# Optimization experiments

Measured on AMD Instinct MI355X. Metric: run time of the kernel, lower is better.

Reference implementation:

```python
import jax, jax.numpy as jnp
import numpy as np

B, H, W, C = 16, 56, 56, 256
K = 3          # ikernel
G = 8          # group
C4 = C // 4    # ratio=4
EPS = 1e-5


def setup_inputs() -> dict:
    key = jax.random.key(0)
    ks = jax.random.split(key, 16)
    s = lambda *sh: 1.0 / np.sqrt(sh[-1])
    inp = {
        'x': jax.random.normal(ks[0], (B, H, W, C), jnp.float32),
        # Involution: conv1 (C->C4, 1x1), BN affine, conv2 (C4 -> G*K*K, 1x1)
        'conv1_w': jax.random.normal(ks[1], (C4, C), jnp.float32) * s(C4, C),
        'conv1_b': jnp.zeros((C4,), jnp.float32),
        'bn_gamma': jnp.ones((C4,), jnp.float32),
        'bn_beta': jnp.zeros((C4,), jnp.float32),
        'conv2_w': jax.random.normal(ks[2], (G * K * K, C4), jnp.float32) * s(G * K * K, C4),
        'conv2_b': jnp.zeros((G * K * K,), jnp.float32),
        # mlp_c: Linear(dim, dim, bias=False)
        'mlp_c_w': jax.random.normal(ks[3], (C, C), jnp.float32) * s(C, C),
        # reweight1: Mlp(dim, dim//4, dim*2)
        'fc1_w': jax.random.normal(ks[4], (C4, C), jnp.float32) * s(C4, C),
        'fc1_b': jnp.zeros((C4,), jnp.float32),
        'fc2_w': jax.random.normal(ks[5], (2 * C, C4), jnp.float32) * s(2 * C, C4),
        'fc2_b': jnp.zeros((2 * C,), jnp.float32),
        # projcnn: Conv2d(dim, dim, 1)
        'projcnn_w': jax.random.normal(ks[6], (C, C), jnp.float32) * s(C, C),
        'projcnn_b': jnp.zeros((C,), jnp.float32),
    }
    return inp


def _involution(x, conv1_w, conv1_b, bn_gamma, bn_beta, conv2_w, conv2_b):
    # x: [B,H,W,C] (channels-last equivalent of the torch NCHW path)
    # kernel-generating branch: 1x1 conv -> BN (batch stats, training mode) -> relu -> 1x1 conv
    t = jnp.einsum('bhwc,oc->bhwo', x, conv1_w) + conv1_b          # [B,H,W,C4]
    mu = t.mean(axis=(0, 1, 2))
    var = t.var(axis=(0, 1, 2))
    t = jax.nn.relu(bn_gamma * (t - mu) * jax.lax.rsqrt(var + EPS) + bn_beta)
    w = jnp.einsum('bhwc,oc->bhwo', t, conv2_w) + conv2_b          # [B,H,W,G*K*K]
    w = w.reshape(B, H, W, G, K * K)
    # unfold: pad and stack the K*K shifted views (row-major kernel order, matches torch)
    p = K // 2
    xp = jnp.pad(x, ((0, 0), (p, p), (p, p), (0, 0)))
    patches = jnp.stack([xp[:, i:i + H, j:j + W, :] for i in range(K) for j in range(K)],
                        axis=3)                                     # [B,H,W,KK,C]
    patches = patches.reshape(B, H, W, K * K, G, C // G)
    out = jnp.einsum('bhwkgc,bhwgk->bhwgc', patches, w)             # multiply + sum over kernel dim
    return out.reshape(B, H, W, C)


def reference(x, conv1_w, conv1_b, bn_gamma, bn_beta, conv2_w, conv2_b,
              mlp_c_w, fc1_w, fc1_b, fc2_w, fc2_b, projcnn_w, projcnn_b):
    hw = _involution(x, conv1_w, conv1_b, bn_gamma, bn_beta, conv2_w, conv2_b)  # [B,H,W,C]
    c = jnp.einsum('bhwc,oc->bhwo', x, mlp_c_w)                                  # [B,H,W,C]
    a = (hw + c).mean(axis=(1, 2))                                               # [B,C]
    a = jax.nn.gelu(jnp.einsum('bc,oc->bo', a, fc1_w) + fc1_b, approximate=False)
    a = jnp.einsum('bc,oc->bo', a, fc2_w) + fc2_b                                # [B,2C]
    a = a.reshape(B, C, 2).transpose(2, 0, 1)                                    # [2,B,C]
    a = jax.nn.softmax(a, axis=0)[:, :, None, None, :]                           # [2,B,1,1,C]
    y = hw * a[0] + c * a[1]
    return jnp.einsum('bhwc,oc->bhwo', y, projcnn_w) + projcnn_b
```

## Files before the change

### kernel.cpp

```cpp
#include <hip/hip_runtime.h>
#include <math.h>

#define BB 16
#define HH 56
#define WW 56
#define CC 256
#define O2P 80
#define NPIX 50176
#define HWP 3136

typedef __attribute__((ext_vector_type(4))) float f32x4;
typedef __attribute__((ext_vector_type(8))) short bh8;
typedef __attribute__((ext_vector_type(4))) short bh4;

__device__ inline short f2bf(float f) {
    union { float f; unsigned u; } v; v.f = f;
    unsigned r = (v.u + 0x7fffu + ((v.u >> 16) & 1u)) >> 16;
    return (short)r;
}
__device__ inline float bf2f(short s) {
    union { unsigned u; float f; } v; v.u = ((unsigned)(unsigned short)s) << 16;
    return v.f;
}

__device__ inline void stage_tile(const short* __restrict__ src, int rowBase, int ldk,
                                  int kc, char* smem, int nchunks, int wid, int lane)
{
    for (int ci = wid; ci < nchunks; ci += 4) {
        int row = ci * 8 + (lane >> 3);
        int cb = (lane & 7) ^ (row & 7);
        const short* gp = src + (size_t)(rowBase + row) * ldk + kc + cb * 8;
        __builtin_amdgcn_global_load_lds(
            (const __attribute__((address_space(1))) void*)gp,
            (__attribute__((address_space(3))) void*)(smem + ci * 1024), 16, 0, 0);
    }
}

template<int BN, int AMODE, int OUTBF>
__global__ __launch_bounds__(256) void mgemm(
    const short* __restrict__ Ab,
    const float* __restrict__ Af, const float* __restrict__ scsh,
    const short* __restrict__ Ah, const short* __restrict__ Ac,
    const float* __restrict__ g0, const float* __restrict__ g1,
    const short* __restrict__ Wb, const float* __restrict__ bias,
    void* __restrict__ outp, int K, int O, int ldOut)
{
    constexpr int WN = (BN == 128) ? 2 : 1;
    constexpr int MR = (BN == 128) ? 4 : 2;
    constexpr int NR = BN / (16 * WN);
    constexpr int BCH = BN / 8;

    __shared__ alignas(16) char smA[16384];
    __shared__ alignas(16) char smB[BN * 128];

    const int tid = threadIdx.x;
    const int lane = tid & 63, wid = tid >> 6;
    const int rowBase = blockIdx.x * 128;
    const int ocBase = blockIdx.y * BN;
    const int waveM = (BN == 128) ? (wid >> 1) * 64 : wid * 32;
    const int waveN = (BN == 128) ? (wid & 1) * 64 : 0;

    f32x4 acc[MR][NR];
    #pragma unroll
    for (int m = 0; m < MR; ++m)
        #pragma unroll
        for (int n = 0; n < NR; ++n) acc[m][n] = f32x4{0.f, 0.f, 0.f, 0.f};

    for (int kc = 0; kc < K; kc += 64) {
        if constexpr (AMODE == 0) {
            stage_tile(Ab, rowBase, K, kc, smA, 16, wid, lane);
        } else if constexpr (AMODE == 1) {
            #pragma unroll
            for (int q = tid; q < 2048; q += 256) {
                int row = q >> 4, k4 = (q & 15) * 4;
                f32x4 v = *(const f32x4*)(Af + (size_t)(rowBase + row) * K + kc + k4);
                bh4 o;
                #pragma unroll
                for (int j = 0; j < 4; ++j) {
                    float sc = scsh[kc + k4 + j], sh = scsh[64 + kc + k4 + j];
                    o[j] = f2bf(fmaxf(v[j] * sc + sh, 0.f));
                }
                int byt = row * 128 + (((k4 >> 3) ^ (row & 7)) << 4) + (k4 & 7) * 2;
                *(bh4*)(smA + byt) = o;
            }
        } else {
            #pragma unroll
            for (int q = tid; q < 1024; q += 256) {
                int row = q >> 3, cb = q & 7;
                int n = rowBase + row;
                int b = n / HWP;
                const size_t off = (size_t)n * 256 + kc + cb * 8;
                bh8 h8 = *(const bh8*)(Ah + off);
                bh8 c8 = *(const bh8*)(Ac + off);
                bh8 o;
                #pragma unroll
                for (int j = 0; j < 8; ++j) {
                    float w0 = g0[b * 256 + kc + cb * 8 + j];
                    float w1 = g1[b * 256 + kc + cb * 8 + j];
                    o[j] = f2bf(bf2f(h8[j]) * w0 + bf2f(c8[j]) * w1);
                }
                *(bh8*)(smA + row * 128 + ((cb ^ (row & 7)) << 4)) = o;
            }
        }
        stage_tile(Wb, ocBase, K, kc, smB, BCH, wid, lane);
        __syncthreads();

        #pragma unroll
        for (int ks = 0; ks < 2; ++ks) {
            bh8 aF[MR], bF[NR];
            #pragma unroll
            for (int m = 0; m < MR; ++m) {
                int r = waveM + m * 16 + (lane & 15);
                int cb = ks * 4 + (lane >> 4);
                aF[m] = *(const bh8*)(smA + r * 128 + ((cb ^ (r & 7)) << 4));
            }
            #pragma unroll
            for (int n = 0; n < NR; ++n) {
                int r = waveN + n * 16 + (lane & 15);
                int cb = ks * 4 + (lane >> 4);
                bF[n] = *(const bh8*)(smB + r * 128 + ((cb ^ (r & 7)) << 4));
            }
            #pragma unroll
            for (int m = 0; m < MR; ++m)
                #pragma unroll
                for (int n = 0; n < NR; ++n)
                    acc[m][n] = __builtin_amdgcn_mfma_f32_16x16x32_bf16(
                        aF[m], bF[n], acc[m][n], 0, 0, 0);
        }
        __syncthreads();
    }

    #pragma unroll
    for (int m = 0; m < MR; ++m)
        #pragma unroll
        for (int n = 0; n < NR; ++n)
            #pragma unroll
            for (int j = 0; j < 4; ++j) {
                int r = rowBase + waveM + m * 16 + (lane >> 4) * 4 + j;
                int c = ocBase + waveN + n * 16 + (lane & 15);
                if (c < O) {
                    float v = acc[m][n][j] + (bias ? bias[c] : 0.f);
                    if constexpr (OUTBF)
                        ((short*)outp)[(size_t)r * ldOut + c] = f2bf(v);
                    else
                        ((float*)outp)[(size_t)r * ldOut + c] = v;
                }
            }
}

__global__ __launch_bounds__(256) void cvt_x_kernel(const float* __restrict__ x,
                                                    short* __restrict__ xb)
{
    size_t i = ((size_t)blockIdx.x * 256 + threadIdx.x) * 8;
    f32x4 v0 = *(const f32x4*)(x + i);
    f32x4 v1 = *(const f32x4*)(x + i + 4);
    bh8 o;
    #pragma unroll
    for (int j = 0; j < 4; ++j) { o[j] = f2bf(v0[j]); o[4 + j] = f2bf(v1[j]); }
    *(bh8*)(xb + i) = o;
}

__global__ __launch_bounds__(256) void cvt_w_kernel(
    const float* __restrict__ c1, const float* __restrict__ mc,
    const float* __restrict__ pj, const float* __restrict__ c2,
    short* __restrict__ c1b, short* __restrict__ mcb,
    short* __restrict__ pjb, short* __restrict__ c2b)
{
    int i = blockIdx.x * 256 + threadIdx.x;
    if (i < 16384) c1b[i] = f2bf(c1[i]);
    if (i < 65536) { mcb[i] = f2bf(mc[i]); pjb[i] = f2bf(pj[i]); }
    if (i < O2P * 64) {
        int o = i >> 6, k = i & 63;
        c2b[i] = (o < 72) ? f2bf(c2[o * 64 + k]) : (short)0;
    }
}

__global__ __launch_bounds__(256) void bn_stats_kernel(
    const float* __restrict__ t, float* __restrict__ stats)
{
    __shared__ float ps[4][64], pq[4][64];
    const int tid = threadIdx.x;
    const int ch = tid & 63, rg = tid >> 6;
    const size_t base = (size_t)blockIdx.x * 512;
    float s = 0.f, q = 0.f;
    for (int r = rg; r < 512; r += 4) {
        float v = t[(base + r) * 64 + ch];
        s += v; q += v * v;
    }
    ps[rg][ch] = s; pq[rg][ch] = q;
    __syncthreads();
    if (rg == 0) {
        atomicAdd(&stats[ch],      ps[0][ch] + ps[1][ch] + ps[2][ch] + ps[3][ch]);
        atomicAdd(&stats[64 + ch], pq[0][ch] + pq[1][ch] + pq[2][ch] + pq[3][ch]);
    }
}

__global__ void bn_finalize_kernel(
    const float* __restrict__ stats, const float* __restrict__ gamma,
    const float* __restrict__ beta, float* __restrict__ scsh)
{
    int ch = threadIdx.x;
    const float invN = 1.f / (float)NPIX;
    float mean = stats[ch] * invN;
    float var  = stats[64 + ch] * invN - mean * mean;
    float sc = gamma[ch] * rsqrtf(var + 1e-5f);
    scsh[ch] = sc;
    scsh[64 + ch] = beta[ch] - mean * sc;
}

__global__ __launch_bounds__(256) void invol_kernel(
    const float* __restrict__ x, const float* __restrict__ wmat,
    short* __restrict__ hwb)
{
    const int bh = blockIdx.x;
    const int b = bh / HH, h = bh % HH;
    const int c = threadIdx.x;
    const int g = c >> 5;
    const float* xb_ = x + (size_t)b * HWP * CC + c;

    float c0[3], c1[3], c2[3];
    auto loadcol = [&](int W, float* dst) {
        if (W < 0 || W >= WW) { dst[0] = dst[1] = dst[2] = 0.f; return; }
        #pragma unroll
        for (int i = 0; i < 3; ++i) {
            int hh = h + i - 1;
            dst[i] = (hh < 0 || hh >= HH) ? 0.f : xb_[((size_t)hh * WW + W) * CC];
        }
    };
    loadcol(-1, c0);
    loadcol(0, c1);
    for (int w = 0; w < WW; ++w) {
        loadcol(w + 1, c2);
        const int n = bh * WW + w;
        const float* wr = wmat + (size_t)n * O2P + g * 9;
        float acc = c0[0] * wr[0] + c1[0] * wr[1] + c2[0] * wr[2]
                  + c0[1] * wr[3] + c1[1] * wr[4] + c2[1] * wr[5]
                  + c0[2] * wr[6] + c1[2] * wr[7] + c2[2] * wr[8];
        hwb[(size_t)n * CC + c] = f2bf(acc);
        c0[0] = c1[0]; c0[1] = c1[1]; c0[2] = c1[2];
        c1[0] = c2[0]; c1[1] = c2[1]; c1[2] = c2[2];
    }
}

__global__ __launch_bounds__(256) void mean_kernel(
    const short* __restrict__ hwb, const short* __restrict__ cmb,
    float* __restrict__ asum)
{
    const int b = blockIdx.x, s = blockIdx.y;
    const int c = threadIdx.x;
    const int base = b * HWP + s * (HWP / 8);
    float acc = 0.f;
    for (int p = 0; p < HWP / 8; ++p) {
        size_t idx = (size_t)(base + p) * CC + c;
        acc += bf2f(hwb[idx]) + bf2f(cmb[idx]);
    }
    atomicAdd(&asum[b * CC + c], acc);
}

__global__ __launch_bounds__(256) void mlp_kernel(
    const float* __restrict__ asum,
    const float* __restrict__ fc1_w, const float* __restrict__ fc1_b,
    const float* __restrict__ fc2_w, const float* __restrict__ fc2_b,
    float* __restrict__ a0, float* __restrict__ a1)
{
    __shared__ float a[256], hbuf[64], f[512];
    const int b = blockIdx.x, tid = threadIdx.x;
    a[tid] = asum[b * CC + tid] * (1.f / (float)HWP);
    __syncthreads();
    if (tid < 64) {
        float s = fc1_b[tid];
        for (int c = 0; c < 256; ++c) s += a[c] * fc1_w[tid * 256 + c];
        hbuf[tid] = 0.5f * s * (1.f + erff(s * 0.7071067811865476f));
    }
    __syncthreads();
    for (int o = tid; o < 512; o += 256) {
        float s = fc2_b[o];
        for (int c = 0; c < 64; ++c) s += hbuf[c] * fc2_w[o * 64 + c];
        f[o] = s;
    }
    __syncthreads();
    float f0 = f[2 * tid], f1 = f[2 * tid + 1];
    float m = fmaxf(f0, f1);
    float e0 = expf(f0 - m), e1 = expf(f1 - m);
    float inv = 1.f / (e0 + e1);
    a0[b * CC + tid] = e0 * inv;
    a1[b * CC + tid] = e1 * inv;
}

extern "C" void kernel_launch(void* const* d_in, const int* in_sizes, int n_in,
                              void* d_out, int out_size, void* d_ws, size_t ws_size,
                              hipStream_t stream)
{
    (void)in_sizes; (void)n_in; (void)out_size; (void)ws_size;
    const float* x        = (const float*)d_in[0];
    const float* conv1_w  = (const float*)d_in[1];
    const float* conv1_b  = (const float*)d_in[2];
    const float* bn_gamma = (const float*)d_in[3];
    const float* bn_beta  = (const float*)d_in[4];
    const float* conv2_w  = (const float*)d_in[5];
    const float* conv2_b  = (const float*)d_in[6];
    const float* mlp_c_w  = (const float*)d_in[7];
    const float* fc1_w    = (const float*)d_in[8];
    const float* fc1_b    = (const float*)d_in[9];
    const float* fc2_w    = (const float*)d_in[10];
    const float* fc2_b    = (const float*)d_in[11];
    const float* projcnn_w= (const float*)d_in[12];
    const float* projcnn_b= (const float*)d_in[13];
    float* out = (float*)d_out;

    char* p = (char*)d_ws;
    short* xb  = (short*)p; p += (size_t)NPIX * 256 * 2;
    short* hwb = (short*)p; p += (size_t)NPIX * 256 * 2;
    short* cmb = (short*)p;
    float* t   = (float*)cmb;
    p += (size_t)NPIX * 256 * 2;
    float* wmat = (float*)p; p += (size_t)NPIX * O2P * 4;
    short* c1b = (short*)p; p += 64 * 256 * 2;
    short* mcb = (short*)p; p += 256 * 256 * 2;
    short* pjb = (short*)p; p += 256 * 256 * 2;
    short* c2b = (short*)p; p += O2P * 64 * 2;
    float* stats = (float*)p; p += 128 * 4;
    float* asum  = (float*)p; p += BB * 256 * 4;
    float* scsh  = (float*)p; p += 128 * 4;
    float* a0    = (float*)p; p += BB * 256 * 4;
    float* a1    = (float*)p; p += BB * 256 * 4;

    hipMemsetAsync(stats, 0, (128 + BB * 256) * sizeof(float), stream);

    cvt_x_kernel<<<NPIX * 256 / (256 * 8), 256, 0, stream>>>(x, xb);
    cvt_w_kernel<<<256, 256, 0, stream>>>(conv1_w, mlp_c_w, projcnn_w, conv2_w,
                                          c1b, mcb, pjb, c2b);
    mgemm<64, 0, 0><<<dim3(392, 1), 256, 0, stream>>>(
        xb, nullptr, nullptr, nullptr, nullptr, nullptr, nullptr,
        c1b, conv1_b, t, 256, 64, 64);
    bn_stats_kernel<<<98, 256, 0, stream>>>(t, stats);
    bn_finalize_kernel<<<1, 64, 0, stream>>>(stats, bn_gamma, bn_beta, scsh);
    mgemm<O2P, 1, 0><<<dim3(392, 1), 256, 0, stream>>>(
        nullptr, t, scsh, nullptr, nullptr, nullptr, nullptr,
        c2b, conv2_b, wmat, 64, 72, O2P);
    invol_kernel<<<BB * HH, 256, 0, stream>>>(x, wmat, hwb);
    mgemm<128, 0, 1><<<dim3(392, 2), 256, 0, stream>>>(
        xb, nullptr, nullptr, nullptr, nullptr, nullptr, nullptr,
        mcb, nullptr, cmb, 256, 256, 256);
    mean_kernel<<<dim3(BB, 8), 256, 0, stream>>>(hwb, cmb, asum);
    mlp_kernel<<<BB, 256, 0, stream>>>(asum, fc1_w, fc1_b, fc2_w, fc2_b, a0, a1);
    mgemm<128, 2, 0><<<dim3(392, 2), 256, 0, stream>>>(
        nullptr, nullptr, nullptr, hwb, cmb, a0, a1,
        pjb, projcnn_b, out, 256, 256, 256);
}
```

Measured before the change: 337.4 us.

## Fuse channel means into conversion and involution, store intermediates in bf16

Removes the separate mean pass over hwb and cmb. The per-batch mean of the mlp_c branch is now computed algebraically from per-batch sums of x, taken during the bf16 conversion and multiplied by mlp_c_w inside the MLP kernel. The involution mean is accumulated inside a restructured involution kernel, which now reads bf16 x and bf16 kernel weights and handles 4 channels per thread over half-row blocks. The conv1 output t and the generated kernels wmat are stored in bf16 rather than fp32, cutting intermediate traffic at the cost of some precision and extra atomics.

Result: faster. 296.4 us (-12.2%).

```diff
diff --git a/kernel.cpp b/kernel.cpp
--- a/kernel.cpp
+++ b/kernel.cpp
@@ -39,7 +39,7 @@
 template<int BN, int AMODE, int OUTBF>
 __global__ __launch_bounds__(256) void mgemm(
     const short* __restrict__ Ab,
-    const float* __restrict__ Af, const float* __restrict__ scsh,
+    const short* __restrict__ At, const float* __restrict__ scsh,
     const short* __restrict__ Ah, const short* __restrict__ Ac,
     const float* __restrict__ g0, const float* __restrict__ g1,
     const short* __restrict__ Wb, const float* __restrict__ bias,
@@ -71,17 +71,16 @@
             stage_tile(Ab, rowBase, K, kc, smA, 16, wid, lane);
         } else if constexpr (AMODE == 1) {
             #pragma unroll
-            for (int q = tid; q < 2048; q += 256) {
-                int row = q >> 4, k4 = (q & 15) * 4;
-                f32x4 v = *(const f32x4*)(Af + (size_t)(rowBase + row) * K + kc + k4);
-                bh4 o;
+            for (int q = tid; q < 1024; q += 256) {
+                int row = q >> 3, cb = q & 7;
+                bh8 v = *(const bh8*)(At + (size_t)(rowBase + row) * K + kc + cb * 8);
+                bh8 o;
                 #pragma unroll
-                for (int j = 0; j < 4; ++j) {
-                    float sc = scsh[kc + k4 + j], sh = scsh[64 + kc + k4 + j];
-                    o[j] = f2bf(fmaxf(v[j] * sc + sh, 0.f));
+                for (int j = 0; j < 8; ++j) {
+                    int k = kc + cb * 8 + j;
+                    o[j] = f2bf(fmaxf(bf2f(v[j]) * scsh[k] + scsh[64 + k], 0.f));
                 }
-                int byt = row * 128 + (((k4 >> 3) ^ (row & 7)) << 4) + (k4 & 7) * 2;
-                *(bh4*)(smA + byt) = o;
+                *(bh8*)(smA + row * 128 + ((cb ^ (row & 7)) << 4)) = o;
             }
         } else {
             #pragma unroll
@@ -149,15 +148,33 @@
 }
 
 __global__ __launch_bounds__(256) void cvt_x_kernel(const float* __restrict__ x,
-                                                    short* __restrict__ xb)
-{
-    size_t i = ((size_t)blockIdx.x * 256 + threadIdx.x) * 8;
-    f32x4 v0 = *(const f32x4*)(x + i);
-    f32x4 v1 = *(const f32x4*)(x + i + 4);
+                                                    short* __restrict__ xb,
+                                                    float* __restrict__ sxb)
+{
+    __shared__ float sm[8][256];
+    const int tid = threadIdx.x;
+    size_t base = (size_t)blockIdx.x * 2048 + tid * 8;
+    const int b = (int)(base >> 8) / HWP;
+    const int ch0 = (int)(base & 255);
+    const int pix = (tid * 8) >> 8;
+
+    f32x4 v0 = *(const f32x4*)(x + base);
+    f32x4 v1 = *(const f32x4*)(x + base + 4);
     bh8 o;
     #pragma unroll
     for (int j = 0; j < 4; ++j) { o[j] = f2bf(v0[j]); o[4 + j] = f2bf(v1[j]); }
-    *(bh8*)(xb + i) = o;
+    *(bh8*)(xb + base) = o;
+
+    #pragma unroll
+    for (int j = 0; j < 4; ++j) {
+        sm[pix][ch0 + j] = v0[j];
+        sm[pix][ch0 + 4 + j] = v1[j];
+    }
+    __syncthreads();
+    float s = 0.f;
+    #pragma unroll
+    for (int p = 0; p < 8; ++p) s += sm[p][tid];
+    atomicAdd(&sxb[b * CC + tid], s);
 }
 
 __global__ __launch_bounds__(256) void cvt_w_kernel(
@@ -176,22 +193,30 @@
 }
 
 __global__ __launch_bounds__(256) void bn_stats_kernel(
-    const float* __restrict__ t, float* __restrict__ stats)
-{
-    __shared__ float ps[4][64], pq[4][64];
+    const short* __restrict__ t, float* __restrict__ stats)
+{
+    __shared__ float ss[32][64], sq[32][64];
     const int tid = threadIdx.x;
-    const int ch = tid & 63, rg = tid >> 6;
-    const size_t base = (size_t)blockIdx.x * 512;
-    float s = 0.f, q = 0.f;
-    for (int r = rg; r < 512; r += 4) {
-        float v = t[(base + r) * 64 + ch];
-        s += v; q += v * v;
-    }
-    ps[rg][ch] = s; pq[rg][ch] = q;
-    __syncthreads();
-    if (rg == 0) {
-        atomicAdd(&stats[ch],      ps[0][ch] + ps[1][ch] + ps[2][ch] + ps[3][ch]);
-        atomicAdd(&stats[64 + ch], pq[0][ch] + pq[1][ch] + pq[2][ch] + pq[3][ch]);
+    const int grp = tid >> 3, ch0 = (tid & 7) * 8;
+    const size_t rowBase = (size_t)blockIdx.x * 512;
+    float s[8] = {}, q[8] = {};
+    for (int r = grp; r < 512; r += 32) {
+        bh8 v = *(const bh8*)(t + (rowBase + r) * 64 + ch0);
+        #pragma unroll
+        for (int j = 0; j < 8; ++j) {
+            float f = bf2f(v[j]);
+            s[j] += f; q[j] += f * f;
+        }
+    }
+    #pragma unroll
+    for (int j = 0; j < 8; ++j) { ss[grp][ch0 + j] = s[j]; sq[grp][ch0 + j] = q[j]; }
+    __syncthreads();
+    if (tid < 64) {
+        float ts = 0.f, tq = 0.f;
+        #pragma unroll
+        for (int g = 0; g < 32; ++g) { ts += ss[g][tid]; tq += sq[g][tid]; }
+        atomicAdd(&stats[tid], ts);
+        atomicAdd(&stats[64 + tid], tq);
     }
 }
 
@@ -209,63 +234,80 @@
 }
 
 __global__ __launch_bounds__(256) void invol_kernel(
-    const float* __restrict__ x, const float* __restrict__ wmat,
-    short* __restrict__ hwb)
-{
-    const int bh = blockIdx.x;
+    const short* __restrict__ xb, const short* __restrict__ wmatb,
+    short* __restrict__ hwb, float* __restrict__ asum)
+{
+    __shared__ float sm4[4][256];
+    const int idx = blockIdx.x;
+    const int s = idx & 1, bh = idx >> 1;
     const int b = bh / HH, h = bh % HH;
-    const int c = threadIdx.x;
-    const int g = c >> 5;
-    const float* xb_ = x + (size_t)b * HWP * CC + c;
-
-    float c0[3], c1[3], c2[3];
-    auto loadcol = [&](int W, float* dst) {
-        if (W < 0 || W >= WW) { dst[0] = dst[1] = dst[2] = 0.f; return; }
+    const int tid = threadIdx.x;
+    const int lane = tid & 63, wid = tid >> 6;
+    const int c4 = lane * 4;
+    const int g = lane >> 3;
+    const int w0 = s * 28 + wid * 7;
+    const short* xbase = xb + ((size_t)b * HWP) * CC + c4;
+
+    float cL[3][4], cM[3][4], cR[3][4];
+    auto loadcol = [&](int Wc, float d[3][4]) {
         #pragma unroll
         for (int i = 0; i < 3; ++i) {
             int hh = h + i - 1;
-            dst[i] = (hh < 0 || hh >= HH) ? 0.f : xb_[((size_t)hh * WW + W) * CC];
+            if (Wc < 0 || Wc >= WW || hh < 0 || hh >= HH) {
+                d[i][0] = d[i][1] = d[i][2] = d[i][3] = 0.f;
+            } else {
+                bh4 v = *(const bh4*)(xbase + (size_t)(hh * WW + Wc) * CC);
+                #pragma unroll
+                for (int j = 0; j < 4; ++j) d[i][j] = bf2f(v[j]);
+            }
         }
     };
-    loadcol(-1, c0);
-    loadcol(0, c1);
-    for (int w = 0; w < WW; ++w) {
-        loadcol(w + 1, c2);
+    loadcol(w0 - 1, cL);
+    loadcol(w0, cM);
+
+    float loc[4] = {0.f, 0.f, 0.f, 0.f};
+    for (int w = w0; w < w0 + 7; ++w) {
+        loadcol(w + 1, cR);
         const int n = bh * WW + w;
-        const float* wr = wmat + (size_t)n * O2P + g * 9;
-        float acc = c0[0] * wr[0] + c1[0] * wr[1] + c2[0] * wr[2]
-                  + c0[1] * wr[3] + c1[1] * wr[4] + c2[1] * wr[5]
-                  + c0[2] * wr[6] + c1[2] * wr[7] + c2[2] * wr[8];
-        hwb[(size_t)n * CC + c] = f2bf(acc);
-        c0[0] = c1[0]; c0[1] = c1[1]; c0[2] = c1[2];
-        c1[0] = c2[0]; c1[1] = c2[1]; c1[2] = c2[2];
-    }
-}
-
-__global__ __launch_bounds__(256) void mean_kernel(
-    const short* __restrict__ hwb, const short* __restrict__ cmb,
-    float* __restrict__ asum)
-{
-    const int b = blockIdx.x, s = blockIdx.y;
-    const int c = threadIdx.x;
-    const int base = b * HWP + s * (HWP / 8);
-    float acc = 0.f;
-    for (int p = 0; p < HWP / 8; ++p) {
-        size_t idx = (size_t)(base + p) * CC + c;
-        acc += bf2f(hwb[idx]) + bf2f(cmb[idx]);
-    }
-    atomicAdd(&asum[b * CC + c], acc);
+        const short* wr = wmatb + (size_t)n * O2P + g * 9;
+        float wf[9];
+        #pragma unroll
+        for (int t9 = 0; t9 < 9; ++t9) wf[t9] = bf2f(wr[t9]);
+        bh4 ov;
+        #pragma unroll
+        for (int j = 0; j < 4; ++j) {
+            float a = cL[0][j] * wf[0] + cM[0][j] * wf[1] + cR[0][j] * wf[2]
+                    + cL[1][j] * wf[3] + cM[1][j] * wf[4] + cR[1][j] * wf[5]
+                    + cL[2][j] * wf[6] + cM[2][j] * wf[7] + cR[2][j] * wf[8];
+            loc[j] += a;
+            ov[j] = f2bf(a);
+        }
+        *(bh4*)(hwb + (size_t)n * CC + c4) = ov;
+        #pragma unroll
+        for (int i = 0; i < 3; ++i)
+            #pragma unroll
+            for (int j = 0; j < 4; ++j) { cL[i][j] = cM[i][j]; cM[i][j] = cR[i][j]; }
+    }
+    #pragma unroll
+    for (int j = 0; j < 4; ++j) sm4[wid][c4 + j] = loc[j];
+    __syncthreads();
+    float tot = sm4[0][tid] + sm4[1][tid] + sm4[2][tid] + sm4[3][tid];
+    atomicAdd(&asum[b * CC + tid], tot);
 }
 
 __global__ __launch_bounds__(256) void mlp_kernel(
-    const float* __restrict__ asum,
+    const float* __restrict__ asum, const float* __restrict__ sxb,
+    const float* __restrict__ mlp_c_w,
     const float* __restrict__ fc1_w, const float* __restrict__ fc1_b,
     const float* __restrict__ fc2_w, const float* __restrict__ fc2_b,
     float* __restrict__ a0, float* __restrict__ a1)
 {
     __shared__ float a[256], hbuf[64], f[512];
     const int b = blockIdx.x, tid = threadIdx.x;
-    a[tid] = asum[b * CC + tid] * (1.f / (float)HWP);
+    float acm = 0.f;
+    const float* wrow = mlp_c_w + (size_t)tid * 256;
+    for (int c = 0; c < 256; ++c) acm += sxb[b * CC + c] * wrow[c];
+    a[tid] = (asum[b * CC + tid] + acm) * (1.f / (float)HWP);
     __syncthreads();
     if (tid < 64) {
         float s = fc1_b[tid];
@@ -312,38 +354,39 @@
     short* xb  = (short*)p; p += (size_t)NPIX * 256 * 2;
     short* hwb = (short*)p; p += (size_t)NPIX * 256 * 2;
     short* cmb = (short*)p;
-    float* t   = (float*)cmb;
+    short* t   = (short*)cmb;
     p += (size_t)NPIX * 256 * 2;
-    float* wmat = (float*)p; p += (size_t)NPIX * O2P * 4;
+    short* wmatb = (short*)p; p += (size_t)NPIX * O2P * 2;
     short* c1b = (short*)p; p += 64 * 256 * 2;
     short* mcb = (short*)p; p += 256 * 256 * 2;
     short* pjb = (short*)p; p += 256 * 256 * 2;
     short* c2b = (short*)p; p += O2P * 64 * 2;
     float* stats = (float*)p; p += 128 * 4;
     float* asum  = (float*)p; p += BB * 256 * 4;
+    float* sxb   = (float*)p; p += BB * 256 * 4;
     float* scsh  = (float*)p; p += 128 * 4;
     float* a0    = (float*)p; p += BB * 256 * 4;
     float* a1    = (float*)p; p += BB * 256 * 4;
 
-    hipMemsetAsync(stats, 0, (128 + BB * 256) * sizeof(float), stream);
-
-    cvt_x_kernel<<<NPIX * 256 / (256 * 8), 256, 0, stream>>>(x, xb);
+    hipMemsetAsync(stats, 0, (128 + 2 * BB * 256) * sizeof(float), stream);
+
+    cvt_x_kernel<<<NPIX * 256 / 2048, 256, 0, stream>>>(x, xb, sxb);
     cvt_w_kernel<<<256, 256, 0, stream>>>(conv1_w, mlp_c_w, projcnn_w, conv2_w,
                                           c1b, mcb, pjb, c2b);
-    mgemm<64, 0, 0><<<dim3(392, 1), 256, 0, stream>>>(
+    mgemm<64, 0, 1><<<dim3(392, 1), 256, 0, stream>>>(
         xb, nullptr, nullptr, nullptr, nullptr, nullptr, nullptr,
         c1b, conv1_b, t, 256, 64, 64);
     bn_stats_kernel<<<98, 256, 0, stream>>>(t, stats);
     bn_finalize_kernel<<<1, 64, 0, stream>>>(stats, bn_gamma, bn_beta, scsh);
-    mgemm<O2P, 1, 0><<<dim3(392, 1), 256, 0, stream>>>(
+    mgemm<O2P, 1, 1><<<dim3(392, 1), 256, 0, stream>>>(
         nullptr, t, scsh, nullptr, nullptr, nullptr, nullptr,
-        c2b, conv2_b, wmat, 64, 72, O2P);
-    invol_kernel<<<BB * HH, 256, 0, stream>>>(x, wmat, hwb);
+        c2b, conv2_b, wmatb, 64, 72, O2P);
+    invol_kernel<<<BB * HH * 2, 256, 0, stream>>>(xb, wmatb, hwb, asum);
     mgemm<128, 0, 1><<<dim3(392, 2), 256, 0, stream>>>(
         xb, nullptr, nullptr, nullptr, nullptr, nullptr, nullptr,
         mcb, nullptr, cmb, 256, 256, 256);
-    mean_kernel<<<dim3(BB, 8), 256, 0, stream>>>(hwb, cmb, asum);
-    mlp_kernel<<<BB, 256, 0, stream>>>(asum, fc1_w, fc1_b, fc2_w, fc2_b, a0, a1);
+    mlp_kernel<<<BB, 256, 0, stream>>>(asum, sxb, mlp_c_w,
+                                       fc1_w, fc1_b, fc2_w, fc2_b, a0, a1);
     mgemm<128, 2, 0><<<dim3(392, 2), 256, 0, stream>>>(
         nullptr, nullptr, nullptr, hwb, cmb, a0, a1,
         pjb, projcnn_b, out, 256, 256, 256);
```
